# Optimization experiments

Hardware: AMD Instinct MI355X
Metric: run time of the kernel (lower is better)

The kernel has to match this reference:

```python
import jax, jax.numpy as jnp
import numpy as np


def setup_inputs() -> dict:
    key = jax.random.key(0)
    ks = jax.random.split(key, 6)
    B, L, F, C, H, D1 = 262144, 20, 7, 16, 16, 8
    s = 0.1
    return {
        "x": jax.random.normal(ks[0], (B, L, F), dtype=jnp.float32),
        "conv_w": jax.random.normal(ks[1], (3, F, C), dtype=jnp.float32) * s,
        "conv_b": jnp.zeros((C,), dtype=jnp.float32),
        "rnn_w": jax.random.normal(ks[2], (C, H), dtype=jnp.float32) * s,
        "rnn_u": jax.random.normal(ks[3], (H, H), dtype=jnp.float32) * s,
        "rnn_b": jnp.zeros((H,), dtype=jnp.float32),
        "d1_w": jax.random.normal(ks[4], (H, D1), dtype=jnp.float32) * s,
        "d1_b": jnp.zeros((D1,), dtype=jnp.float32),
        "out_w": jax.random.normal(ks[5], (D1, 1), dtype=jnp.float32) * s,
        "out_b": jnp.zeros((1,), dtype=jnp.float32),
    }


def reference(x, conv_w, conv_b, rnn_w, rnn_u, rnn_b, d1_w, d1_b, out_w, out_b):
    # Conv1D, kernel 3, 'same' padding, relu.  x: [B,L,F] -> [B,L,C]
    h = jax.lax.conv_general_dilated(
        x, conv_w, window_strides=(1,), padding="SAME",
        dimension_numbers=("NWC", "WIO", "NWC"))
    h = jax.nn.relu(h + conv_b)

    # SimpleRNN(16), tanh, return last state.  Precompute input projections.
    xw = jnp.einsum("blc,ch->blh", h, rnn_w) + rnn_b  # [B,L,H]
    xw_t = jnp.swapaxes(xw, 0, 1)                      # [L,B,H]

    def step(state, xt):
        new = jnp.tanh(xt + state @ rnn_u)
        return new, None

    h0 = jnp.zeros((x.shape[0], rnn_u.shape[0]), dtype=x.dtype)
    h_last, _ = jax.lax.scan(step, h0, xw_t)           # [B,H]

    z = jax.nn.relu(h_last @ d1_w + d1_b)              # [B,8]
    return z @ out_w + out_b                           # [B,1]
```

## Files before the change

### kernel.cpp

```cpp
#include <hip/hip_runtime.h>


#define BLK 64
#define LSEQ 20
#define EPW 84
#define LOG2E2 2.8853900817779268f

typedef _Float16 f16;
typedef __fp16   fp16x2 __attribute__((ext_vector_type(2)));
typedef _Float16 f16x4 __attribute__((ext_vector_type(4)));
typedef _Float16 f16x8 __attribute__((ext_vector_type(8)));
typedef float    f32x4 __attribute__((ext_vector_type(4)));

union UB128 { uint4 q; f16x8 v; };
union UB64  { f16x4 v; fp16x2 p[2]; };
union HU    { fp16x2 p; uint u; };

__global__ __launch_bounds__(BLK, 4) void hybrid_fwd(
    const float* __restrict__ x,
    const float* __restrict__ conv_w, const float* __restrict__ conv_b,
    const float* __restrict__ rnn_w,  const float* __restrict__ rnn_u,
    const float* __restrict__ rnn_b,
    const float* __restrict__ d1_w,   const float* __restrict__ d1_b,
    const float* __restrict__ out_w,  const float* __restrict__ out_b,
    float* __restrict__ out)
{
    __shared__ __align__(16) uint xs[32 * EPW + 8];

    const int lane = threadIdx.x;
    const int b16  = lane & 15, g = lane >> 4;
    const long BE  = (long)blockIdx.x * 32;

    f16x8 A1;
    #pragma unroll
    for (int t = 0; t < 8; ++t) {
        float wv = conv_w[min(g * 7 + t, 20) * 16 + b16];
        float sel = (g < 3 && t < 7) ? wv
                  : ((g == 3 && t == 7) ? conv_b[b16] : 0.f);
        A1[t] = (f16)sel;
    }
    f16x4 A2, AU;
    f32x4 rbp;
    #pragma unroll
    for (int t = 0; t < 4; ++t) {
        A2[t]  = (f16)(LOG2E2 * rnn_w[(4 * g + t) * 16 + b16]);
        AU[t]  = (f16)(LOG2E2 * rnn_u[(4 * g + t) * 16 + b16]);
        rbp[t] = LOG2E2 * rnn_b[4 * g + t];
    }
    f16x4 A3;
    f32x4 c3;
    #pragma unroll
    for (int t = 0; t < 4; ++t) {
        int j = 4 * g + t;
        A3[t] = (f16)(b16 < 8 ? d1_w[j * 8 + b16] : 0.f);
        c3[t] = d1_b[min(j, 7)];
    }
    float ow[4];
    #pragma unroll
    for (int r = 0; r < 4; ++r)
        ow[r] = (g < 2) ? out_w[min(4 * g + r, 7)] : 0.f;
    const float ob = out_b[0];
    const f32x4 zero4 = {0.f, 0.f, 0.f, 0.f};

    const uint4 PAD = make_uint4(0u, 0u, 0u, 0x3C000000u);
    const int e = lane & 31;
    const int h = lane >> 5;
    if (h == 0) *(uint4*)(xs + e * EPW) = PAD;
    if (lane < 2) *(uint4*)(xs + 32 * EPW + 4 * lane) = PAD;

    {
        const float2* sp = (const float2*)(x + (BE + e) * 140 + h * 70);
        float2 f2[35];
        #pragma unroll
        for (int i = 0; i < 35; ++i) f2[i] = sp[i];
        const float* f = (const float*)f2;
        uint* eb = xs + e * EPW;
        #pragma unroll
        for (int i = 0; i < 10; ++i) {
            HU h0, h1, h2, h3;
            h0.p = __builtin_amdgcn_cvt_pkrtz(f[7 * i + 0], f[7 * i + 1]);
            h1.p = __builtin_amdgcn_cvt_pkrtz(f[7 * i + 2], f[7 * i + 3]);
            h2.p = __builtin_amdgcn_cvt_pkrtz(f[7 * i + 4], f[7 * i + 5]);
            h3.p = __builtin_amdgcn_cvt_pkrtz(f[7 * i + 6], 1.0f);
            uint4 val; val.x = h0.u; val.y = h1.u; val.z = h2.u; val.w = h3.u;
            *(uint4*)(eb + 4 * (10 * h + i + 1)) = val;
        }
    }

    asm volatile("s_waitcnt lgkmcnt(0)" ::: "memory");
    __builtin_amdgcn_sched_barrier(0);

    const uint* rb0 = xs + b16 * EPW + 4 * g;
    const uint* rb1 = rb0 + 16 * EPW;

    f16x4 B2sA[LSEQ], B2sB[LSEQ];
    #pragma unroll
    for (int l = 0; l < LSEQ; ++l) {
        UB128 B1a, B1b;
        B1a.q = *(const uint4*)(rb0 + 4 * l);
        B1b.q = *(const uint4*)(rb1 + 4 * l);
        f32x4 a1a = __builtin_amdgcn_mfma_f32_16x16x32_f16(A1, B1a.v, zero4, 0, 0, 0);
        f32x4 a1b = __builtin_amdgcn_mfma_f32_16x16x32_f16(A1, B1b.v, zero4, 0, 0, 0);
        UB64 Ba, Bb;
        Ba.p[0] = __builtin_amdgcn_cvt_pkrtz(fmaxf(a1a[0], 0.f), fmaxf(a1a[1], 0.f));
        Ba.p[1] = __builtin_amdgcn_cvt_pkrtz(fmaxf(a1a[2], 0.f), fmaxf(a1a[3], 0.f));
        Bb.p[0] = __builtin_amdgcn_cvt_pkrtz(fmaxf(a1b[0], 0.f), fmaxf(a1b[1], 0.f));
        Bb.p[1] = __builtin_amdgcn_cvt_pkrtz(fmaxf(a1b[2], 0.f), fmaxf(a1b[3], 0.f));
        B2sA[l] = Ba.v;
        B2sB[l] = Bb.v;
    }

    f16x4 H0 = {}, H1 = {};
    #pragma unroll
    for (int l = 0; l < LSEQ; ++l) {
        f32x4 a20 = __builtin_amdgcn_mfma_f32_16x16x16f16(A2, B2sA[l], rbp, 0, 0, 0);
        f32x4 a21 = __builtin_amdgcn_mfma_f32_16x16x16f16(A2, B2sB[l], rbp, 0, 0, 0);
        a20 = __builtin_amdgcn_mfma_f32_16x16x16f16(AU, H0, a20, 0, 0, 0);
        a21 = __builtin_amdgcn_mfma_f32_16x16x16f16(AU, H1, a21, 0, 0, 0);
        float t00 = __builtin_amdgcn_rcpf(1.f + __builtin_amdgcn_exp2f(a20[0]));
        float t01 = __builtin_amdgcn_rcpf(1.f + __builtin_amdgcn_exp2f(a20[1]));
        float t02 = __builtin_amdgcn_rcpf(1.f + __builtin_amdgcn_exp2f(a20[2]));
        float t03 = __builtin_amdgcn_rcpf(1.f + __builtin_amdgcn_exp2f(a20[3]));
        float t10 = __builtin_amdgcn_rcpf(1.f + __builtin_amdgcn_exp2f(a21[0]));
        float t11 = __builtin_amdgcn_rcpf(1.f + __builtin_amdgcn_exp2f(a21[1]));
        float t12 = __builtin_amdgcn_rcpf(1.f + __builtin_amdgcn_exp2f(a21[2]));
        float t13 = __builtin_amdgcn_rcpf(1.f + __builtin_amdgcn_exp2f(a21[3]));
        UB64 Hn0, Hn1;
        Hn0.p[0] = __builtin_amdgcn_cvt_pkrtz(fmaf(-2.f, t00, 1.f), fmaf(-2.f, t01, 1.f));
        Hn0.p[1] = __builtin_amdgcn_cvt_pkrtz(fmaf(-2.f, t02, 1.f), fmaf(-2.f, t03, 1.f));
        Hn1.p[0] = __builtin_amdgcn_cvt_pkrtz(fmaf(-2.f, t10, 1.f), fmaf(-2.f, t11, 1.f));
        Hn1.p[1] = __builtin_amdgcn_cvt_pkrtz(fmaf(-2.f, t12, 1.f), fmaf(-2.f, t13, 1.f));
        H0 = Hn0.v;
        H1 = Hn1.v;
    }

    f32x4 a30 = __builtin_amdgcn_mfma_f32_16x16x16f16(A3, H0, c3, 0, 0, 0);
    f32x4 a31 = __builtin_amdgcn_mfma_f32_16x16x16f16(A3, H1, c3, 0, 0, 0);
    float p0 = 0.f, p1 = 0.f;
    #pragma unroll
    for (int r = 0; r < 4; ++r) {
        p0 = fmaf(fmaxf(a30[r], 0.f), ow[r], p0);
        p1 = fmaf(fmaxf(a31[r], 0.f), ow[r], p1);
    }
    p0 += __shfl_xor(p0, 16); p0 += __shfl_xor(p0, 32);
    p1 += __shfl_xor(p1, 16); p1 += __shfl_xor(p1, 32);
    if (lane < 16) {
        out[BE + b16]      = p0 + ob;
        out[BE + 16 + b16] = p1 + ob;
    }
}

extern "C" void kernel_launch(void* const* d_in, const int* in_sizes, int n_in,
                              void* d_out, int out_size, void* d_ws, size_t ws_size,
                              hipStream_t stream) {
    const float* x      = (const float*)d_in[0];
    const float* conv_w = (const float*)d_in[1];
    const float* conv_b = (const float*)d_in[2];
    const float* rnn_w  = (const float*)d_in[3];
    const float* rnn_u  = (const float*)d_in[4];
    const float* rnn_b  = (const float*)d_in[5];
    const float* d1_w   = (const float*)d_in[6];
    const float* d1_b   = (const float*)d_in[7];
    const float* out_w  = (const float*)d_in[8];
    const float* out_b  = (const float*)d_in[9];
    float* out = (float*)d_out;

    const int B = out_size;
    const int grid = B / 32;
    hybrid_fwd<<<grid, BLK, 0, stream>>>(x, conv_w, conv_b, rnn_w, rnn_u, rnn_b,
                                         d1_w, d1_b, out_w, out_b, out);
}
```

Baseline: 39.74 us.

## Process two tiles per block, prefetching the second tile's input during compute

Each block now handles 64 batch elements as two 32-element tiles. The global loads for the second tile are issued into registers before the first tile's conv/RNN compute, then written to LDS afterwards. The goal is to hide global memory latency behind the MFMA and transcendental work. In exchange, register pressure rises (launch bounds relaxed to 2) and the grid is halved, which may reduce occupancy.

```diff
diff --git a/kernel.cpp b/kernel.cpp
--- a/kernel.cpp
+++ b/kernel.cpp
@@ -16,7 +16,7 @@
 union UB64  { f16x4 v; fp16x2 p[2]; };
 union HU    { fp16x2 p; uint u; };
 
-__global__ __launch_bounds__(BLK, 4) void hybrid_fwd(
+__global__ __launch_bounds__(BLK, 2) void hybrid_fwd(
     const float* __restrict__ x,
     const float* __restrict__ conv_w, const float* __restrict__ conv_b,
     const float* __restrict__ rnn_w,  const float* __restrict__ rnn_u,
@@ -29,7 +29,10 @@
 
     const int lane = threadIdx.x;
     const int b16  = lane & 15, g = lane >> 4;
-    const long BE  = (long)blockIdx.x * 32;
+    const long BE  = (long)blockIdx.x * 64;
+
+    const int e = lane & 31;
+    const int h = lane >> 5;
 
     f16x8 A1;
     #pragma unroll
@@ -63,91 +66,112 @@
     const f32x4 zero4 = {0.f, 0.f, 0.f, 0.f};
 
     const uint4 PAD = make_uint4(0u, 0u, 0u, 0x3C000000u);
-    const int e = lane & 31;
-    const int h = lane >> 5;
     if (h == 0) *(uint4*)(xs + e * EPW) = PAD;
     if (lane < 2) *(uint4*)(xs + 32 * EPW + 4 * lane) = PAD;
 
-    {
-        const float2* sp = (const float2*)(x + (BE + e) * 140 + h * 70);
-        float2 f2[35];
-        #pragma unroll
-        for (int i = 0; i < 35; ++i) f2[i] = sp[i];
-        const float* f = (const float*)f2;
-        uint* eb = xs + e * EPW;
-        #pragma unroll
-        for (int i = 0; i < 10; ++i) {
-            HU h0, h1, h2, h3;
-            h0.p = __builtin_amdgcn_cvt_pkrtz(f[7 * i + 0], f[7 * i + 1]);
-            h1.p = __builtin_amdgcn_cvt_pkrtz(f[7 * i + 2], f[7 * i + 3]);
-            h2.p = __builtin_amdgcn_cvt_pkrtz(f[7 * i + 4], f[7 * i + 5]);
-            h3.p = __builtin_amdgcn_cvt_pkrtz(f[7 * i + 6], 1.0f);
-            uint4 val; val.x = h0.u; val.y = h1.u; val.z = h2.u; val.w = h3.u;
-            *(uint4*)(eb + 4 * (10 * h + i + 1)) = val;
-        }
+    float2 f2[35];
+
+#define LOADF2(T)                                                              \
+    {                                                                          \
+        const float2* sp = (const float2*)(x + (BE + (T) * 32 + e) * 140 + h * 70); \
+        _Pragma("unroll")                                                      \
+        for (int i = 0; i < 35; ++i) f2[i] = sp[i];                            \
     }
 
-    asm volatile("s_waitcnt lgkmcnt(0)" ::: "memory");
+#define WRITETILE()                                                            \
+    {                                                                          \
+        const float* f = (const float*)f2;                                     \
+        uint* eb = xs + e * EPW;                                               \
+        _Pragma("unroll")                                                      \
+        for (int i = 0; i < 10; ++i) {                                         \
+            HU h0, h1, h2, h3;                                                 \
+            h0.p = __builtin_amdgcn_cvt_pkrtz(f[7 * i + 0], f[7 * i + 1]);     \
+            h1.p = __builtin_amdgcn_cvt_pkrtz(f[7 * i + 2], f[7 * i + 3]);     \
+            h2.p = __builtin_amdgcn_cvt_pkrtz(f[7 * i + 4], f[7 * i + 5]);     \
+            h3.p = __builtin_amdgcn_cvt_pkrtz(f[7 * i + 6], 1.0f);             \
+            uint4 val; val.x = h0.u; val.y = h1.u; val.z = h2.u; val.w = h3.u; \
+            *(uint4*)(eb + 4 * (10 * h + i + 1)) = val;                        \
+        }                                                                      \
+    }
+
+#define FENCE()                                                                \
+    asm volatile("s_waitcnt lgkmcnt(0)" ::: "memory");                         \
     __builtin_amdgcn_sched_barrier(0);
 
     const uint* rb0 = xs + b16 * EPW + 4 * g;
     const uint* rb1 = rb0 + 16 * EPW;
 
-    f16x4 B2sA[LSEQ], B2sB[LSEQ];
-    #pragma unroll
-    for (int l = 0; l < LSEQ; ++l) {
-        UB128 B1a, B1b;
-        B1a.q = *(const uint4*)(rb0 + 4 * l);
-        B1b.q = *(const uint4*)(rb1 + 4 * l);
-        f32x4 a1a = __builtin_amdgcn_mfma_f32_16x16x32_f16(A1, B1a.v, zero4, 0, 0, 0);
-        f32x4 a1b = __builtin_amdgcn_mfma_f32_16x16x32_f16(A1, B1b.v, zero4, 0, 0, 0);
-        UB64 Ba, Bb;
-        Ba.p[0] = __builtin_amdgcn_cvt_pkrtz(fmaxf(a1a[0], 0.f), fmaxf(a1a[1], 0.f));
-        Ba.p[1] = __builtin_amdgcn_cvt_pkrtz(fmaxf(a1a[2], 0.f), fmaxf(a1a[3], 0.f));
-        Bb.p[0] = __builtin_amdgcn_cvt_pkrtz(fmaxf(a1b[0], 0.f), fmaxf(a1b[1], 0.f));
-        Bb.p[1] = __builtin_amdgcn_cvt_pkrtz(fmaxf(a1b[2], 0.f), fmaxf(a1b[3], 0.f));
-        B2sA[l] = Ba.v;
-        B2sB[l] = Bb.v;
-    }
+    auto compute_tile = [&](int tidx) {
+        f16x4 B2sA[LSEQ], B2sB[LSEQ];
+        #pragma unroll
+        for (int l = 0; l < LSEQ; ++l) {
+            UB128 B1a, B1b;
+            B1a.q = *(const uint4*)(rb0 + 4 * l);
+            B1b.q = *(const uint4*)(rb1 + 4 * l);
+            f32x4 a1a = __builtin_amdgcn_mfma_f32_16x16x32_f16(A1, B1a.v, zero4, 0, 0, 0);
+            f32x4 a1b = __builtin_amdgcn_mfma_f32_16x16x32_f16(A1, B1b.v, zero4, 0, 0, 0);
+            UB64 Ba, Bb;
+            Ba.p[0] = __builtin_amdgcn_cvt_pkrtz(fmaxf(a1a[0], 0.f), fmaxf(a1a[1], 0.f));
+            Ba.p[1] = __builtin_amdgcn_cvt_pkrtz(fmaxf(a1a[2], 0.f), fmaxf(a1a[3], 0.f));
+            Bb.p[0] = __builtin_amdgcn_cvt_pkrtz(fmaxf(a1b[0], 0.f), fmaxf(a1b[1], 0.f));
+            Bb.p[1] = __builtin_amdgcn_cvt_pkrtz(fmaxf(a1b[2], 0.f), fmaxf(a1b[3], 0.f));
+            B2sA[l] = Ba.v;
+            B2sB[l] = Bb.v;
+        }
+        f16x4 H0 = {}, H1 = {};
+        #pragma unroll
+        for (int l = 0; l < LSEQ; ++l) {
+            f32x4 a20 = __builtin_amdgcn_mfma_f32_16x16x16f16(A2, B2sA[l], rbp, 0, 0, 0);
+            f32x4 a21 = __builtin_amdgcn_mfma_f32_16x16x16f16(A2, B2sB[l], rbp, 0, 0, 0);
+            a20 = __builtin_amdgcn_mfma_f32_16x16x16f16(AU, H0, a20, 0, 0, 0);
+            a21 = __builtin_amdgcn_mfma_f32_16x16x16f16(AU, H1, a21, 0, 0, 0);
+            float t00 = __builtin_amdgcn_rcpf(1.f + __builtin_amdgcn_exp2f(a20[0]));
+            float t01 = __builtin_amdgcn_rcpf(1.f + __builtin_amdgcn_exp2f(a20[1]));
+            float t02 = __builtin_amdgcn_rcpf(1.f + __builtin_amdgcn_exp2f(a20[2]));
+            float t03 = __builtin_amdgcn_rcpf(1.f + __builtin_amdgcn_exp2f(a20[3]));
+            float t10 = __builtin_amdgcn_rcpf(1.f + __builtin_amdgcn_exp2f(a21[0]));
+            float t11 = __builtin_amdgcn_rcpf(1.f + __builtin_amdgcn_exp2f(a21[1]));
+            float t12 = __builtin_amdgcn_rcpf(1.f + __builtin_amdgcn_exp2f(a21[2]));
+            float t13 = __builtin_amdgcn_rcpf(1.f + __builtin_amdgcn_exp2f(a21[3]));
+            UB64 Hn0, Hn1;
+            Hn0.p[0] = __builtin_amdgcn_cvt_pkrtz(fmaf(-2.f, t00, 1.f), fmaf(-2.f, t01, 1.f));
+            Hn0.p[1] = __builtin_amdgcn_cvt_pkrtz(fmaf(-2.f, t02, 1.f), fmaf(-2.f, t03, 1.f));
+            Hn1.p[0] = __builtin_amdgcn_cvt_pkrtz(fmaf(-2.f, t10, 1.f), fmaf(-2.f, t11, 1.f));
+            Hn1.p[1] = __builtin_amdgcn_cvt_pkrtz(fmaf(-2.f, t12, 1.f), fmaf(-2.f, t13, 1.f));
+            H0 = Hn0.v;
+            H1 = Hn1.v;
+        }
+        f32x4 a30 = __builtin_amdgcn_mfma_f32_16x16x16f16(A3, H0, c3, 0, 0, 0);
+        f32x4 a31 = __builtin_amdgcn_mfma_f32_16x16x16f16(A3, H1, c3, 0, 0, 0);
+        float p0 = 0.f, p1 = 0.f;
+        #pragma unroll
+        for (int r = 0; r < 4; ++r) {
+            p0 = fmaf(fmaxf(a30[r], 0.f), ow[r], p0);
+            p1 = fmaf(fmaxf(a31[r], 0.f), ow[r], p1);
+        }
+        p0 += __shfl_xor(p0, 16); p0 += __shfl_xor(p0, 32);
+        p1 += __shfl_xor(p1, 16); p1 += __shfl_xor(p1, 32);
+        if (lane < 16) {
+            out[BE + tidx * 32 + b16]      = p0 + ob;
+            out[BE + tidx * 32 + 16 + b16] = p1 + ob;
+        }
+    };
 
-    f16x4 H0 = {}, H1 = {};
-    #pragma unroll
-    for (int l = 0; l < LSEQ; ++l) {
-        f32x4 a20 = __builtin_amdgcn_mfma_f32_16x16x16f16(A2, B2sA[l], rbp, 0, 0, 0);
-        f32x4 a21 = __builtin_amdgcn_mfma_f32_16x16x16f16(A2, B2sB[l], rbp, 0, 0, 0);
-        a20 = __builtin_amdgcn_mfma_f32_16x16x16f16(AU, H0, a20, 0, 0, 0);
-        a21 = __builtin_amdgcn_mfma_f32_16x16x16f16(AU, H1, a21, 0, 0, 0);
-        float t00 = __builtin_amdgcn_rcpf(1.f + __builtin_amdgcn_exp2f(a20[0]));
-        float t01 = __builtin_amdgcn_rcpf(1.f + __builtin_amdgcn_exp2f(a20[1]));
-        float t02 = __builtin_amdgcn_rcpf(1.f + __builtin_amdgcn_exp2f(a20[2]));
-        float t03 = __builtin_amdgcn_rcpf(1.f + __builtin_amdgcn_exp2f(a20[3]));
-        float t10 = __builtin_amdgcn_rcpf(1.f + __builtin_amdgcn_exp2f(a21[0]));
-        float t11 = __builtin_amdgcn_rcpf(1.f + __builtin_amdgcn_exp2f(a21[1]));
-        float t12 = __builtin_amdgcn_rcpf(1.f + __builtin_amdgcn_exp2f(a21[2]));
-        float t13 = __builtin_amdgcn_rcpf(1.f + __builtin_amdgcn_exp2f(a21[3]));
-        UB64 Hn0, Hn1;
-        Hn0.p[0] = __builtin_amdgcn_cvt_pkrtz(fmaf(-2.f, t00, 1.f), fmaf(-2.f, t01, 1.f));
-        Hn0.p[1] = __builtin_amdgcn_cvt_pkrtz(fmaf(-2.f, t02, 1.f), fmaf(-2.f, t03, 1.f));
-        Hn1.p[0] = __builtin_amdgcn_cvt_pkrtz(fmaf(-2.f, t10, 1.f), fmaf(-2.f, t11, 1.f));
-        Hn1.p[1] = __builtin_amdgcn_cvt_pkrtz(fmaf(-2.f, t12, 1.f), fmaf(-2.f, t13, 1.f));
-        H0 = Hn0.v;
-        H1 = Hn1.v;
-    }
+    LOADF2(0);
+    WRITETILE();
+    FENCE();
 
-    f32x4 a30 = __builtin_amdgcn_mfma_f32_16x16x16f16(A3, H0, c3, 0, 0, 0);
-    f32x4 a31 = __builtin_amdgcn_mfma_f32_16x16x16f16(A3, H1, c3, 0, 0, 0);
-    float p0 = 0.f, p1 = 0.f;
-    #pragma unroll
-    for (int r = 0; r < 4; ++r) {
-        p0 = fmaf(fmaxf(a30[r], 0.f), ow[r], p0);
-        p1 = fmaf(fmaxf(a31[r], 0.f), ow[r], p1);
-    }
-    p0 += __shfl_xor(p0, 16); p0 += __shfl_xor(p0, 32);
-    p1 += __shfl_xor(p1, 16); p1 += __shfl_xor(p1, 32);
-    if (lane < 16) {
-        out[BE + b16]      = p0 + ob;
-        out[BE + 16 + b16] = p1 + ob;
-    }
+    LOADF2(1);
+    compute_tile(0);
+
+    FENCE();
+    WRITETILE();
+    FENCE();
+    compute_tile(1);
+
+#undef LOADF2
+#undef WRITETILE
+#undef FENCE
 }
 
 extern "C" void kernel_launch(void* const* d_in, const int* in_sizes, int n_in,
@@ -166,7 +190,7 @@
     float* out = (float*)d_out;
 
     const int B = out_size;
-    const int grid = B / 32;
+    const int grid = B / 64;
     hybrid_fwd<<<grid, BLK, 0, stream>>>(x, conv_w, conv_b, rnn_w, rnn_u, rnn_b,
                                          d1_w, d1_b, out_w, out_b, out);
 }
```

Result: slower. 45.66 us (+14.9%).
